# Optimization experiments

Measured on AMD Instinct MI355X. Metric: run time of the kernel, lower is better.

The kernel has to match this reference:

```python
import jax, jax.numpy as jnp
import numpy as np

K = 16  # number of piecewise-linear intervals (fixed in params_set)


def setup_inputs() -> dict:
    key = jax.random.key(0)
    k1, k2 = jax.random.split(key)
    B, S, D = 4, 4096, 2048
    x = jax.random.normal(k1, (B, S, D), dtype=jnp.float32)
    threshold = jnp.ones((1,), dtype=jnp.float32)          # alpha > 0
    theta = 0.1 * jax.random.normal(k2, (K,), dtype=jnp.float32)
    dst = jnp.arange(K, dtype=jnp.float32) / K             # delta * arange(K), delta = 1/K
    return {
        "x": x,
        "threshold": threshold,
        "theta": theta,
        "dst": dst,
        "Qn": 0,
        "Qp": 15,                 # 2**4 - 1 (activation, num_bits=4)
        "num_elements": B * S * D,
    }


def reference(x, threshold, theta, dst, Qn, Qp, num_elements):
    # LCQ_quantizer.forward (non 2-bit-weight path) -> LCQ_fast_core.forward
    s = float(Qp)
    theta_tmp = jax.nn.softmax(theta)                       # softmax over dim 0
    gamma = theta_tmp * K                                   # theta_tmp / delta
    beta = jnp.concatenate(
        [jnp.zeros((1,), theta_tmp.dtype), jnp.cumsum(theta_tmp)[: K - 1]]
    )
    alpha = threshold                                       # shape (1,), broadcasts

    flag_middle = (jnp.abs(x) < alpha).astype(x.dtype)
    flag_high = 1.0 - flag_middle
    x_tmp = jnp.abs(x) / alpha

    # compress: searchsorted bin lookup + piecewise affine
    idx = jnp.searchsorted(dst, x_tmp, side="right")        # in [1, K]
    y = gamma[idx - 1] * (x_tmp - dst[idx - 1]) + beta[idx - 1]
    y_q = jnp.round(y * s) / s                              # uniform round-quantize

    # expand: second searchsorted + inverse affine
    idx_q = jnp.searchsorted(beta, y_q, side="right")       # in [1, K]
    z_mid = (y_q - beta[idx_q - 1]) / gamma[idx_q - 1] + dst[idx_q - 1]

    z = jnp.sign(x) * alpha * (z_mid * flag_middle + flag_high)
    return z
```

## Files before the change

kernel.cpp:

```cpp
#include <hip/hip_runtime.h>
#include <math.h>

#define KB 16

__device__ __forceinline__ float lcq_one(float xv, float alpha,
                                         const float* __restrict__ s_gamma,
                                         const float* __restrict__ s_beta,
                                         const float* __restrict__ s_zval)
{
    float a  = fabsf(xv);
    float xt = __fdiv_rn(a, alpha);
    float t16 = __fmul_rn(xt, 16.0f);
    int   j  = (int)fminf(t16, 15.0f);
    float gj = s_gamma[j];
    float bj = s_beta[j];
    float dj = (float)j * 0.0625f;
    float y  = __fadd_rn(__fmul_rn(gj, __fsub_rn(xt, dj)), bj);
    float t  = rintf(__fmul_rn(y, 15.0f));
    int   m  = (int)fminf(fmaxf(t, 0.0f), 15.0f);
    float v  = (a < alpha) ? s_zval[m] : 1.0f;
    float r  = __fmul_rn(alpha, v);
    return (xv > 0.0f) ? r : (xv < 0.0f ? -r : 0.0f);
}

__global__ __launch_bounds__(256) void lcq_kernel(
    const float* __restrict__ x,
    const float* __restrict__ thr,
    const float* __restrict__ theta,
    float* __restrict__ out,
    long long n)
{
    __shared__ float s_gamma[KB];
    __shared__ float s_beta[KB];
    __shared__ float s_zval[KB];
    __shared__ float s_alpha;

    if (threadIdx.x == 0) {
        float th[KB];
        float mx = theta[0];
        th[0] = mx;
        #pragma unroll
        for (int i = 1; i < KB; ++i) { th[i] = theta[i]; mx = fmaxf(mx, th[i]); }
        float ex[KB];
        float sum = 0.0f;
        #pragma unroll
        for (int i = 0; i < KB; ++i) { ex[i] = expf(__fsub_rn(th[i], mx)); sum = __fadd_rn(sum, ex[i]); }
        float sm[KB];
        #pragma unroll
        for (int i = 0; i < KB; ++i) sm[i] = __fdiv_rn(ex[i], sum);

        float beta[KB], gamma[KB];
        beta[0] = 0.0f;
        float c = sm[0];
        #pragma unroll
        for (int i = 1; i < KB; ++i) { beta[i] = c; c = __fadd_rn(c, sm[i]); }
        #pragma unroll
        for (int i = 0; i < KB; ++i) gamma[i] = __fmul_rn(sm[i], 16.0f);

        #pragma unroll
        for (int i = 0; i < KB; ++i) { s_gamma[i] = gamma[i]; s_beta[i] = beta[i]; }

        for (int m = 0; m < KB; ++m) {
            float yq = __fdiv_rn((float)m, 15.0f);
            int iq = 0;
            #pragma unroll
            for (int i = 1; i < KB; ++i) iq += (beta[i] <= yq) ? 1 : 0;
            s_zval[m] = __fadd_rn(__fdiv_rn(__fsub_rn(yq, beta[iq]), gamma[iq]),
                                  (float)iq * 0.0625f);
        }
        s_alpha = thr[0];
    }
    __syncthreads();

    const float alpha = s_alpha;

    long long tid      = (long long)blockIdx.x * blockDim.x + threadIdx.x;
    long long nthreads = (long long)gridDim.x * blockDim.x;
    long long n4       = n >> 2;

    const float4* __restrict__ x4 = (const float4*)x;
    float4* __restrict__ o4 = (float4*)out;

    for (long long i = tid; i < n4; i += nthreads) {
        float4 v = x4[i];
        float4 r;
        r.x = lcq_one(v.x, alpha, s_gamma, s_beta, s_zval);
        r.y = lcq_one(v.y, alpha, s_gamma, s_beta, s_zval);
        r.z = lcq_one(v.z, alpha, s_gamma, s_beta, s_zval);
        r.w = lcq_one(v.w, alpha, s_gamma, s_beta, s_zval);
        o4[i] = r;
    }
    for (long long i = (n4 << 2) + tid; i < n; i += nthreads) {
        out[i] = lcq_one(x[i], alpha, s_gamma, s_beta, s_zval);
    }
}

extern "C" void kernel_launch(void* const* d_in, const int* in_sizes, int n_in,
                              void* d_out, int out_size, void* d_ws, size_t ws_size,
                              hipStream_t stream) {
    const float* x     = (const float*)d_in[0];
    const float* thr   = (const float*)d_in[1];
    const float* theta = (const float*)d_in[2];
    float* out = (float*)d_out;

    long long n = (long long)in_sizes[0];
    dim3 block(256);
    dim3 grid(2048);
    hipLaunchKernelGGL(lcq_kernel, grid, block, 0, stream, x, thr, theta, out, n);
}
```

Measured before the change: 244.7 us.

## Unroll grid-stride loop with nontemporal loads and stores, use reciprocal alpha

The grid-stride loop now issues four independent 16-byte nontemporal loads and stores per iteration, which raises memory-level parallelism and bypasses cache retention for streamed data. The per-element division by alpha becomes a multiply by a reciprocal computed once. Gamma and beta are packed into one float2 LDS array so a single read fetches both, and the sign handling is simplified to copysignf. Multiplying by the reciprocal can differ from true division in the last bit, which may shift bin or rounding decisions for a few elements.

```diff
diff --git a/kernel.cpp b/kernel.cpp
--- a/kernel.cpp
+++ b/kernel.cpp
@@ -3,24 +3,25 @@
 
 #define KB 16
 
-__device__ __forceinline__ float lcq_one(float xv, float alpha,
-                                         const float* __restrict__ s_gamma,
-                                         const float* __restrict__ s_beta,
-                                         const float* __restrict__ s_zval)
+typedef float vf4 __attribute__((ext_vector_type(4)));
+
+__device__ __forceinline__ float lcq_core(float xv, float alpha, float rcp_alpha,
+                                          const float2* __restrict__ s_gb,
+                                          const float* __restrict__ s_zval)
 {
-    float a  = fabsf(xv);
-    float xt = __fdiv_rn(a, alpha);
+    float a   = fabsf(xv);
+    float xt  = __fmul_rn(a, rcp_alpha);
     float t16 = __fmul_rn(xt, 16.0f);
-    int   j  = (int)fminf(t16, 15.0f);
-    float gj = s_gamma[j];
-    float bj = s_beta[j];
-    float dj = (float)j * 0.0625f;
-    float y  = __fadd_rn(__fmul_rn(gj, __fsub_rn(xt, dj)), bj);
-    float t  = rintf(__fmul_rn(y, 15.0f));
-    int   m  = (int)fminf(fmaxf(t, 0.0f), 15.0f);
-    float v  = (a < alpha) ? s_zval[m] : 1.0f;
-    float r  = __fmul_rn(alpha, v);
-    return (xv > 0.0f) ? r : (xv < 0.0f ? -r : 0.0f);
+    float jf  = fminf(t16, 15.0f);
+    int   j   = (int)jf;
+    float2 gb = s_gb[j];
+    float dj  = __fmul_rn(floorf(jf), 0.0625f);
+    float y   = __fadd_rn(__fmul_rn(gb.x, __fsub_rn(xt, dj)), gb.y);
+    float t   = rintf(__fmul_rn(y, 15.0f));
+    int   m   = (int)fminf(t, 15.0f);
+    float v   = (a < alpha) ? s_zval[m] : 1.0f;
+    float r   = __fmul_rn(alpha, v);
+    return copysignf(r, xv);
 }
 
 __global__ __launch_bounds__(256) void lcq_kernel(
@@ -30,10 +31,9 @@
     float* __restrict__ out,
     long long n)
 {
-    __shared__ float s_gamma[KB];
-    __shared__ float s_beta[KB];
-    __shared__ float s_zval[KB];
-    __shared__ float s_alpha;
+    __shared__ float2 s_gb[KB];
+    __shared__ float  s_zval[KB];
+    __shared__ float  s_scal[2];
 
     if (threadIdx.x == 0) {
         float th[KB];
@@ -58,7 +58,7 @@
         for (int i = 0; i < KB; ++i) gamma[i] = __fmul_rn(sm[i], 16.0f);
 
         #pragma unroll
-        for (int i = 0; i < KB; ++i) { s_gamma[i] = gamma[i]; s_beta[i] = beta[i]; }
+        for (int i = 0; i < KB; ++i) s_gb[i] = make_float2(gamma[i], beta[i]);
 
         for (int m = 0; m < KB; ++m) {
             float yq = __fdiv_rn((float)m, 15.0f);
@@ -68,30 +68,61 @@
             s_zval[m] = __fadd_rn(__fdiv_rn(__fsub_rn(yq, beta[iq]), gamma[iq]),
                                   (float)iq * 0.0625f);
         }
-        s_alpha = thr[0];
+        float alpha = thr[0];
+        s_scal[0] = alpha;
+        s_scal[1] = __fdiv_rn(1.0f, alpha);
     }
     __syncthreads();
 
-    const float alpha = s_alpha;
+    const float alpha = s_scal[0];
+    const float rcpa  = s_scal[1];
 
-    long long tid      = (long long)blockIdx.x * blockDim.x + threadIdx.x;
-    long long nthreads = (long long)gridDim.x * blockDim.x;
-    long long n4       = n >> 2;
+    const long long tid = (long long)blockIdx.x * blockDim.x + threadIdx.x;
+    const long long NT  = (long long)gridDim.x * blockDim.x;
+    const long long n4  = n >> 2;
 
-    const float4* __restrict__ x4 = (const float4*)x;
-    float4* __restrict__ o4 = (float4*)out;
+    const vf4* __restrict__ x4 = (const vf4*)x;
+    vf4* __restrict__ o4 = (vf4*)out;
 
-    for (long long i = tid; i < n4; i += nthreads) {
-        float4 v = x4[i];
-        float4 r;
-        r.x = lcq_one(v.x, alpha, s_gamma, s_beta, s_zval);
-        r.y = lcq_one(v.y, alpha, s_gamma, s_beta, s_zval);
-        r.z = lcq_one(v.z, alpha, s_gamma, s_beta, s_zval);
-        r.w = lcq_one(v.w, alpha, s_gamma, s_beta, s_zval);
+    long long i = tid;
+    for (; i + 3 * NT < n4; i += 4 * NT) {
+        vf4 v0 = __builtin_nontemporal_load(&x4[i]);
+        vf4 v1 = __builtin_nontemporal_load(&x4[i + NT]);
+        vf4 v2 = __builtin_nontemporal_load(&x4[i + 2 * NT]);
+        vf4 v3 = __builtin_nontemporal_load(&x4[i + 3 * NT]);
+        vf4 r0, r1, r2, r3;
+        r0.x = lcq_core(v0.x, alpha, rcpa, s_gb, s_zval);
+        r0.y = lcq_core(v0.y, alpha, rcpa, s_gb, s_zval);
+        r0.z = lcq_core(v0.z, alpha, rcpa, s_gb, s_zval);
+        r0.w = lcq_core(v0.w, alpha, rcpa, s_gb, s_zval);
+        r1.x = lcq_core(v1.x, alpha, rcpa, s_gb, s_zval);
+        r1.y = lcq_core(v1.y, alpha, rcpa, s_gb, s_zval);
+        r1.z = lcq_core(v1.z, alpha, rcpa, s_gb, s_zval);
+        r1.w = lcq_core(v1.w, alpha, rcpa, s_gb, s_zval);
+        r2.x = lcq_core(v2.x, alpha, rcpa, s_gb, s_zval);
+        r2.y = lcq_core(v2.y, alpha, rcpa, s_gb, s_zval);
+        r2.z = lcq_core(v2.z, alpha, rcpa, s_gb, s_zval);
+        r2.w = lcq_core(v2.w, alpha, rcpa, s_gb, s_zval);
+        r3.x = lcq_core(v3.x, alpha, rcpa, s_gb, s_zval);
+        r3.y = lcq_core(v3.y, alpha, rcpa, s_gb, s_zval);
+        r3.z = lcq_core(v3.z, alpha, rcpa, s_gb, s_zval);
+        r3.w = lcq_core(v3.w, alpha, rcpa, s_gb, s_zval);
+        __builtin_nontemporal_store(r0, &o4[i]);
+        __builtin_nontemporal_store(r1, &o4[i + NT]);
+        __builtin_nontemporal_store(r2, &o4[i + 2 * NT]);
+        __builtin_nontemporal_store(r3, &o4[i + 3 * NT]);
+    }
+    for (; i < n4; i += NT) {
+        vf4 v = x4[i];
+        vf4 r;
+        r.x = lcq_core(v.x, alpha, rcpa, s_gb, s_zval);
+        r.y = lcq_core(v.y, alpha, rcpa, s_gb, s_zval);
+        r.z = lcq_core(v.z, alpha, rcpa, s_gb, s_zval);
+        r.w = lcq_core(v.w, alpha, rcpa, s_gb, s_zval);
         o4[i] = r;
     }
-    for (long long i = (n4 << 2) + tid; i < n; i += nthreads) {
-        out[i] = lcq_one(x[i], alpha, s_gamma, s_beta, s_zval);
+    for (long long k = (n4 << 2) + tid; k < n; k += NT) {
+        out[k] = lcq_core(x[k], alpha, rcpa, s_gb, s_zval);
     }
 }
 
```

Measured after the change: 244.3 us. Within noise of the previous version (-0.2%).
